# Kernel tuning notes

Measured on AMD Instinct MI355X. Metric: run time of the kernel, lower is better.

The kernel has to match this reference:

```python
import jax, jax.numpy as jnp
import numpy as np

DIM = 1024
DEPTH = 6
HEADS = 16
MLP_DIM = 4096
EPS = 1e-5


def setup_inputs() -> dict:
    key = jax.random.key(0)
    ks = jax.random.split(key, 8)
    d, L, f = DIM, DEPTH, MLP_DIM
    s = lambda fan_in: 1.0 / np.sqrt(fan_in)
    inp = {
        "x": jax.random.normal(ks[0], (4, 1024, d), dtype=jnp.float32),
        "ln1_w": jnp.ones((L, d), jnp.float32),
        "ln1_b": jnp.zeros((L, d), jnp.float32),
        "qkv_w": jax.random.normal(ks[1], (L, d, 3 * d), jnp.float32) * s(d),
        "qkv_b": jnp.zeros((L, 3 * d), jnp.float32),
        "proj_w": jax.random.normal(ks[2], (L, d, d), jnp.float32) * s(d),
        "proj_b": jnp.zeros((L, d), jnp.float32),
        "ln2_w": jnp.ones((L, d), jnp.float32),
        "ln2_b": jnp.zeros((L, d), jnp.float32),
        "mlp_w1": jax.random.normal(ks[3], (L, d, f), jnp.float32) * s(d),
        "mlp_b1": jax.random.normal(ks[4], (L, f), jnp.float32) * 1e-6,
        "mlp_w2": jax.random.normal(ks[5], (L, f, d), jnp.float32) * s(f),
        "mlp_b2": jax.random.normal(ks[6], (L, d), jnp.float32) * 1e-6,
    }
    return inp


def _layer_norm(x, w, b):
    mu = jnp.mean(x, axis=-1, keepdims=True)
    var = jnp.mean(jnp.square(x - mu), axis=-1, keepdims=True)
    return (x - mu) * jax.lax.rsqrt(var + EPS) * w + b


def _block(x, ln1_w, ln1_b, qkv_w, qkv_b, proj_w, proj_b,
           ln2_w, ln2_b, mlp_w1, mlp_b1, mlp_w2, mlp_b2):
    b, n, d = x.shape
    h = HEADS
    hd = d // h
    scale = d ** (-0.5)  # note: original scales by dim**-0.5, not head_dim**-0.5
    # attention sublayer (pre-LN + residual)
    y = _layer_norm(x, ln1_w, ln1_b)
    qkv = y @ qkv_w + qkv_b                      # [b, n, 3d]
    qkv = qkv.reshape(b, n, 3, h, hd)            # matches 'b n (qkv h d)'
    q, k, v = (jnp.moveaxis(qkv[:, :, i], 1, 2) for i in range(3))  # [b, h, n, hd]
    dots = jnp.einsum('bhid,bhjd->bhij', q, k) * scale
    attn = jax.nn.softmax(dots, axis=-1)
    out = jnp.einsum('bhij,bhjd->bhid', attn, v)
    out = jnp.moveaxis(out, 1, 2).reshape(b, n, d)
    x = x + out @ proj_w + proj_b
    # MLP sublayer (pre-LN + residual)
    y = _layer_norm(x, ln2_w, ln2_b)
    y = jax.nn.gelu(y @ mlp_w1 + mlp_b1, approximate=False)
    x = x + y @ mlp_w2 + mlp_b2
    return x


def reference(x, ln1_w, ln1_b, qkv_w, qkv_b, proj_w, proj_b,
              ln2_w, ln2_b, mlp_w1, mlp_b1, mlp_w2, mlp_b2):
    for l in range(DEPTH):
        x = _block(x, ln1_w[l], ln1_b[l], qkv_w[l], qkv_b[l],
                   proj_w[l], proj_b[l], ln2_w[l], ln2_b[l],
                   mlp_w1[l], mlp_b1[l], mlp_w2[l], mlp_b2[l])
    return x
```

## Files before the change

### kernel.cpp

```cpp
#include <hip/hip_runtime.h>

typedef __attribute__((ext_vector_type(8))) short short8;
typedef __attribute__((ext_vector_type(4))) float floatx4;

#define DIM   1024
#define SEQ   1024
#define BATCH 4
#define NHEAD 16
#define HDIM  64
#define MLPD  4096
#define DEPTH 6
#define MTOK  (BATCH*SEQ)

__device__ __forceinline__ unsigned short f2bf(float f) {
    union { float f; unsigned u; } v; v.f = f;
    unsigned r = v.u + 0x7fffu + ((v.u >> 16) & 1u);
    return (unsigned short)(r >> 16);
}

__device__ __forceinline__ void gld16(const void* g, void* l) {
    __builtin_amdgcn_global_load_lds(
        (const __attribute__((address_space(1))) unsigned int*)g,
        (__attribute__((address_space(3))) unsigned int*)l, 16, 0, 0);
}

__global__ __launch_bounds__(256) void ln_kernel(
    const float* __restrict__ x, const float* __restrict__ w,
    const float* __restrict__ b, unsigned short* __restrict__ y)
{
    __shared__ float red[8];
    const int row = blockIdx.x;
    const int t = threadIdx.x;
    const float4 v = ((const float4*)(x + (size_t)row * DIM))[t];
    float s = v.x + v.y + v.z + v.w;
#pragma unroll
    for (int m = 1; m < 64; m <<= 1) s += __shfl_xor(s, m);
    if ((t & 63) == 0) red[t >> 6] = s;
    __syncthreads();
    const float mu = (red[0] + red[1] + red[2] + red[3]) * (1.0f / DIM);
    const float d0 = v.x - mu, d1 = v.y - mu, d2 = v.z - mu, d3 = v.w - mu;
    float q = d0 * d0 + d1 * d1 + d2 * d2 + d3 * d3;
#pragma unroll
    for (int m = 1; m < 64; m <<= 1) q += __shfl_xor(q, m);
    if ((t & 63) == 0) red[4 + (t >> 6)] = q;
    __syncthreads();
    const float var = (red[4] + red[5] + red[6] + red[7]) * (1.0f / DIM);
    const float rs = rsqrtf(var + 1e-5f);
    const float4 wv = ((const float4*)w)[t];
    const float4 bv = ((const float4*)b)[t];
    ushort4 o;
    o.x = f2bf(d0 * rs * wv.x + bv.x);
    o.y = f2bf(d1 * rs * wv.y + bv.y);
    o.z = f2bf(d2 * rs * wv.z + bv.z);
    o.w = f2bf(d3 * rs * wv.w + bv.w);
    ((ushort4*)(y + (size_t)row * DIM))[t] = o;
}

__global__ __launch_bounds__(256) void wtrans_kernel(
    const float* __restrict__ W, unsigned short* __restrict__ Wt, int K, int N)
{
    __shared__ float tile[64][65];
    const int n0 = blockIdx.x * 64, k0 = blockIdx.y * 64;
    const int t = threadIdx.x;
#pragma unroll
    for (int p = t; p < 1024; p += 256) {
        const int k = p >> 4, nq = (p & 15) * 4;
        const float4 v = *(const float4*)&W[(size_t)(k0 + k) * N + n0 + nq];
        tile[k][nq + 0] = v.x; tile[k][nq + 1] = v.y;
        tile[k][nq + 2] = v.z; tile[k][nq + 3] = v.w;
    }
    __syncthreads();
#pragma unroll
    for (int p = t; p < 1024; p += 256) {
        const int n = p >> 4, kq = (p & 15) * 4;
        ushort4 o;
        o.x = f2bf(tile[kq + 0][n]); o.y = f2bf(tile[kq + 1][n]);
        o.z = f2bf(tile[kq + 2][n]); o.w = f2bf(tile[kq + 3][n]);
        *(ushort4*)&Wt[(size_t)(n0 + n) * K + k0 + kq] = o;
    }
}

template <int MODE>
__global__ __launch_bounds__(512, 2) void gemm8(
    const unsigned short* __restrict__ A, const unsigned short* __restrict__ Bt,
    const float* __restrict__ bias, void* __restrict__ Cout,
    int M, int ldk, int Keff, int N)
{
    (void)M;
    __shared__ __align__(16) unsigned short Lds[65536];
    unsigned short* const LA = Lds;
    unsigned short* const LB = Lds + 32768;

    const int bm = blockIdx.y * 256, bn = blockIdx.x * 256;
    const int kz = blockIdx.z;
    const int tid  = threadIdx.x;
    const int lane = tid & 63, wid = tid >> 6;
    const int lm = lane & 15, quad = lane >> 4;
    const int wrow = wid >> 2, wcol = wid & 3;

    const int l8    = lane >> 3;
    const int chunk = (((lane & 7) ^ l8) << 3);
    const int reg0  = wid * 2, reg1 = reg0 + 1;
    const size_t hstep = (size_t)128 * ldk;

    const unsigned short* gA0 = A  + (size_t)kz * Keff + (size_t)(bm + reg0 * 8 + l8) * ldk + chunk;
    const unsigned short* gA1 = A  + (size_t)kz * Keff + (size_t)(bm + reg1 * 8 + l8) * ldk + chunk;
    const unsigned short* gB0 = Bt + (size_t)kz * Keff + (size_t)(bn + reg0 * 8 + l8) * ldk + chunk;
    const unsigned short* gB1 = Bt + (size_t)kz * Keff + (size_t)(bn + reg1 * 8 + l8) * ldk + chunk;

    auto stA = [&](int s, int h, int t) {
        gld16(gA0 + h * hstep + t * 64, LA + s * 16384 + h * 8192 + reg0 * 512);
        gld16(gA1 + h * hstep + t * 64, LA + s * 16384 + h * 8192 + reg1 * 512);
    };
    auto stB = [&](int s, int h, int t) {
        gld16(gB0 + h * hstep + t * 64, LB + s * 16384 + h * 8192 + reg0 * 512);
        gld16(gB1 + h * hstep + t * 64, LB + s * 16384 + h * 8192 + reg1 * 512);
    };

    floatx4 acc[8][4] = {};
    short8 bfr[2][4];

    const int NT = Keff >> 6;

    stA(0, 0, 0); stA(0, 1, 0); stB(0, 0, 0); stB(0, 1, 0);
    stA(1, 0, 1); stB(1, 0, 1); stB(1, 1, 1);
    asm volatile("s_waitcnt vmcnt(6)" ::: "memory");
    __builtin_amdgcn_sched_barrier(0);
    __builtin_amdgcn_s_barrier();

    const int arow0 = wrow * 64 + lm;
    const int brow0 = wcol * 64 + lm;
    const char* const lAc = (const char*)LA;
    const char* const lBc = (const char*)LB;

#define RD(base, sOff, row, cb) \
    (*(const short8*)((base) + (sOff) + (row) * 128 + ((cb) ^ (((row) & 7) << 4))))

    for (int t = 0; t < NT; ++t) {
        const int s = t & 1, s2 = s ^ 1;
        const int sOff = s * 32768;
        short8 af[4];

#pragma unroll
        for (int ti = 0; ti < 4; ti++) af[ti]     = RD(lAc, sOff, arow0 + ti * 16, quad * 16);
#pragma unroll
        for (int ni = 0; ni < 4; ni++) bfr[0][ni] = RD(lBc, sOff, brow0 + ni * 16, quad * 16);
        if (t + 1 < NT) stA(s2, 1, t + 1);
        __builtin_amdgcn_s_barrier();
        asm volatile("s_waitcnt lgkmcnt(0)" ::: "memory");
        __builtin_amdgcn_sched_barrier(0);
        __builtin_amdgcn_s_setprio(1);
#pragma unroll
        for (int ti = 0; ti < 4; ti++)
#pragma unroll
            for (int ni = 0; ni < 4; ni++)
                acc[ti][ni] = __builtin_amdgcn_mfma_f32_16x16x32_bf16(af[ti], bfr[0][ni], acc[ti][ni], 0, 0, 0);
        __builtin_amdgcn_s_setprio(0);
        __builtin_amdgcn_s_barrier();

#pragma unroll
        for (int ti = 0; ti < 4; ti++) af[ti]     = RD(lAc, sOff, arow0 + ti * 16, 64 + quad * 16);
#pragma unroll
        for (int ni = 0; ni < 4; ni++) bfr[1][ni] = RD(lBc, sOff, brow0 + ni * 16, 64 + quad * 16);
        __builtin_amdgcn_s_barrier();
        asm volatile("s_waitcnt lgkmcnt(0)" ::: "memory");
        __builtin_amdgcn_sched_barrier(0);
        __builtin_amdgcn_s_setprio(1);
#pragma unroll
        for (int ti = 0; ti < 4; ti++)
#pragma unroll
            for (int ni = 0; ni < 4; ni++)
                acc[ti][ni] = __builtin_amdgcn_mfma_f32_16x16x32_bf16(af[ti], bfr[1][ni], acc[ti][ni], 0, 0, 0);
        __builtin_amdgcn_s_setprio(0);
        __builtin_amdgcn_s_barrier();

#pragma unroll
        for (int ti = 0; ti < 4; ti++) af[ti] = RD(lAc, sOff, 128 + arow0 + ti * 16, quad * 16);
        if (t + 2 < NT) { stA(s, 0, t + 2); stB(s, 0, t + 2); }
        __builtin_amdgcn_s_barrier();
        asm volatile("s_waitcnt lgkmcnt(0)" ::: "memory");
        __builtin_amdgcn_sched_barrier(0);
        __builtin_amdgcn_s_setprio(1);
#pragma unroll
        for (int ti = 0; ti < 4; ti++)
#pragma unroll
            for (int ni = 0; ni < 4; ni++)
                acc[4 + ti][ni] = __builtin_amdgcn_mfma_f32_16x16x32_bf16(af[ti], bfr[0][ni], acc[4 + ti][ni], 0, 0, 0);
        __builtin_amdgcn_s_setprio(0);
        __builtin_amdgcn_s_barrier();

#pragma unroll
        for (int ti = 0; ti < 4; ti++) af[ti] = RD(lAc, sOff, 128 + arow0 + ti * 16, 64 + quad * 16);
        if (t + 2 < NT) stB(s, 1, t + 2);
        __builtin_amdgcn_s_barrier();
        asm volatile("s_waitcnt lgkmcnt(0)" ::: "memory");
        __builtin_amdgcn_sched_barrier(0);
        __builtin_amdgcn_s_setprio(1);
#pragma unroll
        for (int ti = 0; ti < 4; ti++)
#pragma unroll
            for (int ni = 0; ni < 4; ni++)
                acc[4 + ti][ni] = __builtin_amdgcn_mfma_f32_16x16x32_bf16(af[ti], bfr[1][ni], acc[4 + ti][ni], 0, 0, 0);
        __builtin_amdgcn_s_setprio(0);
        if (t + 2 < NT) { asm volatile("s_waitcnt vmcnt(6)" ::: "memory"); }
        else            { asm volatile("s_waitcnt vmcnt(0)" ::: "memory"); }
        __builtin_amdgcn_sched_barrier(0);
        __builtin_amdgcn_s_barrier();
    }
#undef RD

#pragma unroll
    for (int st = 0; st < 2; st++)
#pragma unroll
        for (int ti = 0; ti < 4; ti++) {
            const int row = bm + st * 128 + wrow * 64 + ti * 16 + quad * 4;
#pragma unroll
            for (int ni = 0; ni < 4; ni++) {
                const int col = bn + wcol * 64 + ni * 16 + lm;
                const float bb = (MODE == 3 && kz != 0) ? 0.0f : bias[col];
                const floatx4 a = acc[st * 4 + ti][ni];
#pragma unroll
                for (int r = 0; r < 4; r++) {
                    float v = a[r] + bb;
                    const size_t idx = (size_t)(row + r) * N + col;
                    if constexpr (MODE == 0) {
                        ((unsigned short*)Cout)[idx] = f2bf(v);
                    } else if constexpr (MODE == 1) {
                        const float g = 0.5f * v * (1.0f + erff(v * 0.70710678118654752f));
                        ((unsigned short*)Cout)[idx] = f2bf(g);
                    } else if constexpr (MODE == 2) {
                        ((float*)Cout)[idx] += v;
                    } else {
                        atomicAdd(&((float*)Cout)[idx], v);
                    }
                }
            }
        }
}

__global__ __launch_bounds__(256) void vtrans_kernel(
    const unsigned short* __restrict__ qkv, unsigned short* __restrict__ Vt)
{
    __shared__ unsigned short tile[64][65];
    const int bh = blockIdx.x, nt = blockIdx.y;
    const int b = bh >> 4, h = bh & 15;
    const int t = threadIdx.x;
#pragma unroll
    for (int p = t; p < 4096; p += 256) {
        const int n = p >> 6, c = p & 63;
        tile[n][c] = qkv[(size_t)(b * SEQ + nt * 64 + n) * (3 * DIM) + 2 * DIM + h * HDIM + c];
    }
    __syncthreads();
#pragma unroll
    for (int p = t; p < 4096; p += 256) {
        const int hd = p >> 6, n = p & 63;
        Vt[((size_t)bh * HDIM + hd) * SEQ + nt * 64 + n] = tile[n][hd];
    }
}

__global__ __launch_bounds__(256) void attn_kernel(
    const unsigned short* __restrict__ qkv, const unsigned short* __restrict__ Vt,
    unsigned short* __restrict__ O)
{
    __shared__ __align__(16) unsigned short P[2][4][32 * 72];
    const int bh = blockIdx.x;
    const int b = bh >> 4, h = bh & 15;
    const int tid = threadIdx.x, lane = tid & 63, wid = tid >> 6;
    const int lm = lane & 15, quad = lane >> 4;
    const int q0 = (blockIdx.y * 4 + wid) * 32;

    const unsigned short* Qbase = qkv + (size_t)(b * SEQ) * (3 * DIM) + h * HDIM;
    const unsigned short* Kbase = Qbase + DIM;
    const unsigned short* Vbase = Vt + (size_t)bh * HDIM * SEQ;

    short8 aq[2][2];
#pragma unroll
    for (int qt = 0; qt < 2; qt++)
#pragma unroll
        for (int t = 0; t < 2; t++)
            aq[qt][t] = *(const short8*)&Qbase[(size_t)(q0 + qt * 16 + lm) * (3 * DIM) + t * 32 + quad * 8];

    short8 ones;
#pragma unroll
    for (int t = 0; t < 8; t++) ones[t] = (short)0x3F80;

    floatx4 o[2][4] = {};
    floatx4 sacc[2] = {};
    const float scale = 0.03125f;
    const float M = 3.0f;

    for (int i = 0; i < SEQ / 64; i++) {
        const int kt = i * 64;
        short8 bk[4][2];
#pragma unroll
        for (int s = 0; s < 4; s++)
#pragma unroll
            for (int t = 0; t < 2; t++)
                bk[s][t] = *(const short8*)&Kbase[(size_t)(kt + s * 16 + lm) * (3 * DIM) + t * 32 + quad * 8];
        short8 bv[4][2];
#pragma unroll
        for (int ht = 0; ht < 4; ht++)
#pragma unroll
            for (int kh = 0; kh < 2; kh++)
                bv[ht][kh] = *(const short8*)&Vbase[(size_t)(ht * 16 + lm) * SEQ + kt + kh * 32 + quad * 8];

        unsigned short* Pw = P[i & 1][wid];
#pragma unroll
        for (int qt = 0; qt < 2; qt++)
#pragma unroll
            for (int s = 0; s < 4; s++) {
                floatx4 sv = {};
                sv = __builtin_amdgcn_mfma_f32_16x16x32_bf16(aq[qt][0], bk[s][0], sv, 0, 0, 0);
                sv = __builtin_amdgcn_mfma_f32_16x16x32_bf16(aq[qt][1], bk[s][1], sv, 0, 0, 0);
#pragma unroll
                for (int r = 0; r < 4; r++)
                    Pw[(qt * 16 + quad * 4 + r) * 72 + s * 16 + lm] =
                        f2bf(__expf(fmaf(sv[r], scale, -M)));
            }
        short8 pa[2][2];
#pragma unroll
        for (int qt = 0; qt < 2; qt++)
#pragma unroll
            for (int kh = 0; kh < 2; kh++)
                pa[qt][kh] = *(const short8*)&Pw[(qt * 16 + lm) * 72 + kh * 32 + quad * 8];
#pragma unroll
        for (int qt = 0; qt < 2; qt++) {
            sacc[qt] = __builtin_amdgcn_mfma_f32_16x16x32_bf16(pa[qt][0], ones, sacc[qt], 0, 0, 0);
            sacc[qt] = __builtin_amdgcn_mfma_f32_16x16x32_bf16(pa[qt][1], ones, sacc[qt], 0, 0, 0);
        }
#pragma unroll
        for (int qt = 0; qt < 2; qt++)
#pragma unroll
            for (int ht = 0; ht < 4; ht++) {
                o[qt][ht] = __builtin_amdgcn_mfma_f32_16x16x32_bf16(pa[qt][0], bv[ht][0], o[qt][ht], 0, 0, 0);
                o[qt][ht] = __builtin_amdgcn_mfma_f32_16x16x32_bf16(pa[qt][1], bv[ht][1], o[qt][ht], 0, 0, 0);
            }
    }

#pragma unroll
    for (int qt = 0; qt < 2; qt++)
#pragma unroll
        for (int r = 0; r < 4; r++) {
            const float inv = 1.0f / sacc[qt][r];
            const int qrow = q0 + qt * 16 + quad * 4 + r;
            const size_t orow = (size_t)(b * SEQ + qrow) * DIM + h * HDIM;
#pragma unroll
            for (int ti = 0; ti < 4; ti++)
                O[orow + ti * 16 + lm] = f2bf(o[qt][ti][r] * inv);
        }
}

extern "C" void kernel_launch(void* const* d_in, const int* in_sizes, int n_in,
                              void* d_out, int out_size, void* d_ws, size_t ws_size,
                              hipStream_t stream)
{
    (void)in_sizes; (void)n_in; (void)out_size; (void)ws_size;
    const float* x      = (const float*)d_in[0];
    const float* ln1_w  = (const float*)d_in[1];
    const float* ln1_b  = (const float*)d_in[2];
    const float* qkv_w  = (const float*)d_in[3];
    const float* qkv_b  = (const float*)d_in[4];
    const float* proj_w = (const float*)d_in[5];
    const float* proj_b = (const float*)d_in[6];
    const float* ln2_w  = (const float*)d_in[7];
    const float* ln2_b  = (const float*)d_in[8];
    const float* mlp_w1 = (const float*)d_in[9];
    const float* mlp_b1 = (const float*)d_in[10];
    const float* mlp_w2 = (const float*)d_in[11];
    const float* mlp_b2 = (const float*)d_in[12];

    char* p = (char*)d_ws;
    float* xbuf = (float*)p;                    p += (size_t)MTOK * DIM * 4;
    unsigned short* y = (unsigned short*)p;     p += (size_t)MTOK * DIM * 2;
    unsigned short* big = (unsigned short*)p;   p += (size_t)MTOK * MLPD * 2;
    unsigned short* Vt = (unsigned short*)p;    p += (size_t)MTOK * DIM * 2;
    unsigned short* attno = (unsigned short*)p; p += (size_t)MTOK * DIM * 2;
    unsigned short* qkvT = (unsigned short*)p;  p += (size_t)DIM * 3 * DIM * 2;
    unsigned short* projT = (unsigned short*)p; p += (size_t)DIM * DIM * 2;
    unsigned short* mlp1T = (unsigned short*)p; p += (size_t)DIM * MLPD * 2;
    unsigned short* mlp2T = (unsigned short*)p; p += (size_t)MLPD * DIM * 2;

    hipMemcpyAsync(xbuf, x, (size_t)MTOK * DIM * 4, hipMemcpyDeviceToDevice, stream);

    for (int l = 0; l < DEPTH; l++) {
        wtrans_kernel<<<dim3(3 * DIM / 64, DIM / 64), 256, 0, stream>>>(
            qkv_w + (size_t)l * DIM * 3 * DIM, qkvT, DIM, 3 * DIM);
        wtrans_kernel<<<dim3(DIM / 64, DIM / 64), 256, 0, stream>>>(
            proj_w + (size_t)l * DIM * DIM, projT, DIM, DIM);
        wtrans_kernel<<<dim3(MLPD / 64, DIM / 64), 256, 0, stream>>>(
            mlp_w1 + (size_t)l * DIM * MLPD, mlp1T, DIM, MLPD);
        wtrans_kernel<<<dim3(DIM / 64, MLPD / 64), 256, 0, stream>>>(
            mlp_w2 + (size_t)l * MLPD * DIM, mlp2T, MLPD, DIM);

        ln_kernel<<<MTOK, 256, 0, stream>>>(xbuf, ln1_w + l * DIM, ln1_b + l * DIM, y);
        gemm8<0><<<dim3(3 * DIM / 256, MTOK / 256), 512, 0, stream>>>(
            y, qkvT, qkv_b + (size_t)l * 3 * DIM, big, MTOK, DIM, DIM, 3 * DIM);
        vtrans_kernel<<<dim3(64, 16), 256, 0, stream>>>(big, Vt);
        attn_kernel<<<dim3(64, 8), 256, 0, stream>>>(big, Vt, attno);
        gemm8<2><<<dim3(DIM / 256, MTOK / 256), 512, 0, stream>>>(
            attno, projT, proj_b + (size_t)l * DIM, xbuf, MTOK, DIM, DIM, DIM);
        ln_kernel<<<MTOK, 256, 0, stream>>>(xbuf, ln2_w + l * DIM, ln2_b + l * DIM, y);
        gemm8<1><<<dim3(MLPD / 256, MTOK / 256), 512, 0, stream>>>(
            y, mlp1T, mlp_b1 + (size_t)l * MLPD, big, MTOK, DIM, DIM, MLPD);
        gemm8<3><<<dim3(DIM / 256, MTOK / 256, 4), 512, 0, stream>>>(
            big, mlp2T, mlp_b2 + (size_t)l * DIM, xbuf, MTOK, MLPD, MLPD / 4, DIM);
    }
    hipMemcpyAsync(d_out, xbuf, (size_t)MTOK * DIM * 4, hipMemcpyDeviceToDevice, stream);
}
```

Measured before the change: 2.185 ms.

## Replace split-K atomics with partial buffers plus reduce; add XCD-aware block remap

The split-K MLP down-projection now writes each K-slice's result to a separate partial buffer instead of atomically adding into the residual. A new reduction kernel then sums the four partials with bias and residual. All GEMM launches also remap the linear workgroup id so that groups of eight consecutive ids spread across the chip's partitions, aiming for better L2 locality. This trades atomic traffic for extra partial-buffer memory traffic, one extra kernel launch, and 64MB of workspace.

```diff
diff --git a/kernel.cpp b/kernel.cpp
--- a/kernel.cpp
+++ b/kernel.cpp
@@ -56,6 +56,29 @@
     ((ushort4*)(y + (size_t)row * DIM))[t] = o;
 }
 
+__global__ __launch_bounds__(256) void reduce4_kernel(
+    const float* __restrict__ p, const float* __restrict__ bias,
+    float* __restrict__ xb)
+{
+    const size_t stride = (size_t)MTOK * DIM / 4;
+#pragma unroll
+    for (int rep = 0; rep < 2; rep++) {
+        const size_t i = (size_t)(blockIdx.x * 2 + rep) * 256 + threadIdx.x;
+        const int c4 = (int)(i & (DIM / 4 - 1));
+        const float4 b4 = ((const float4*)bias)[c4];
+        float4 v = ((const float4*)xb)[i];
+        const float4 a0 = ((const float4*)p)[i];
+        const float4 a1 = ((const float4*)p)[i + stride];
+        const float4 a2 = ((const float4*)p)[i + 2 * stride];
+        const float4 a3 = ((const float4*)p)[i + 3 * stride];
+        v.x += a0.x + a1.x + a2.x + a3.x + b4.x;
+        v.y += a0.y + a1.y + a2.y + a3.y + b4.y;
+        v.z += a0.z + a1.z + a2.z + a3.z + b4.z;
+        v.w += a0.w + a1.w + a2.w + a3.w + b4.w;
+        ((float4*)xb)[i] = v;
+    }
+}
+
 __global__ __launch_bounds__(256) void wtrans_kernel(
     const float* __restrict__ W, unsigned short* __restrict__ Wt, int K, int N)
 {
@@ -86,13 +109,18 @@
     const float* __restrict__ bias, void* __restrict__ Cout,
     int M, int ldk, int Keff, int N)
 {
-    (void)M;
     __shared__ __align__(16) unsigned short Lds[65536];
     unsigned short* const LA = Lds;
     unsigned short* const LB = Lds + 32768;
 
-    const int bm = blockIdx.y * 256, bn = blockIdx.x * 256;
-    const int kz = blockIdx.z;
+    int lin = (blockIdx.z * gridDim.y + blockIdx.y) * gridDim.x + blockIdx.x;
+    const int nwg = gridDim.x * gridDim.y * gridDim.z;
+    lin = (lin & 7) * (nwg >> 3) + (lin >> 3);
+    const int bx = lin % gridDim.x; lin /= gridDim.x;
+    const int by = lin % gridDim.y;
+    const int kz = lin / gridDim.y;
+
+    const int bm = by * 256, bn = bx * 256;
     const int tid  = threadIdx.x;
     const int lane = tid & 63, wid = tid >> 6;
     const int lm = lane & 15, quad = lane >> 4;
@@ -217,7 +245,7 @@
 #pragma unroll
             for (int ni = 0; ni < 4; ni++) {
                 const int col = bn + wcol * 64 + ni * 16 + lm;
-                const float bb = (MODE == 3 && kz != 0) ? 0.0f : bias[col];
+                const float bb = (MODE == 4) ? 0.0f : bias[col];
                 const floatx4 a = acc[st * 4 + ti][ni];
 #pragma unroll
                 for (int r = 0; r < 4; r++) {
@@ -231,7 +259,7 @@
                     } else if constexpr (MODE == 2) {
                         ((float*)Cout)[idx] += v;
                     } else {
-                        atomicAdd(&((float*)Cout)[idx], v);
+                        ((float*)Cout)[(size_t)kz * M * N + idx] = v;
                     }
                 }
             }
@@ -379,6 +407,7 @@
     unsigned short* projT = (unsigned short*)p; p += (size_t)DIM * DIM * 2;
     unsigned short* mlp1T = (unsigned short*)p; p += (size_t)DIM * MLPD * 2;
     unsigned short* mlp2T = (unsigned short*)p; p += (size_t)MLPD * DIM * 2;
+    float* partial = (float*)p;                 p += (size_t)4 * MTOK * DIM * 4;
 
     hipMemcpyAsync(xbuf, x, (size_t)MTOK * DIM * 4, hipMemcpyDeviceToDevice, stream);
 
@@ -402,8 +431,10 @@
         ln_kernel<<<MTOK, 256, 0, stream>>>(xbuf, ln2_w + l * DIM, ln2_b + l * DIM, y);
         gemm8<1><<<dim3(MLPD / 256, MTOK / 256), 512, 0, stream>>>(
             y, mlp1T, mlp_b1 + (size_t)l * MLPD, big, MTOK, DIM, DIM, MLPD);
-        gemm8<3><<<dim3(DIM / 256, MTOK / 256, 4), 512, 0, stream>>>(
-            big, mlp2T, mlp_b2 + (size_t)l * DIM, xbuf, MTOK, MLPD, MLPD / 4, DIM);
+        gemm8<4><<<dim3(DIM / 256, MTOK / 256, 4), 512, 0, stream>>>(
+            big, mlp2T, mlp_b2 + (size_t)l * DIM, partial, MTOK, MLPD, MLPD / 4, DIM);
+        reduce4_kernel<<<2048, 256, 0, stream>>>(
+            partial, mlp_b2 + (size_t)l * DIM, xbuf);
     }
     hipMemcpyAsync(d_out, xbuf, (size_t)MTOK * DIM * 4, hipMemcpyDeviceToDevice, stream);
 }
```

After: 2.426 ms. +11.0%, slower.
